# Kernel tuning notes

Measured on AMD Instinct MI355X. Metric: run time of the kernel, lower is better.

The kernel has to match this reference:

```python
import jax, jax.numpy as jnp
import numpy as np

IN_SIZE = 128
OUT_SIZE = 128
N = IN_SIZE * OUT_SIZE  # num_nets = 16384
H = 5                   # subnetwork hidden width
B = 2048                # batch


def setup_inputs() -> dict:
    key = jax.random.key(0)
    k_x, k0, k1, k2 = jax.random.split(key, 4)
    x = jax.random.normal(k_x, (B, IN_SIZE), dtype=jnp.float32)
    # init scaling mirrors _init_scaled_weights: std*0.1, last layer uses in_dim*input_size
    s0 = np.float32(np.sqrt(2.0 / 1.0) * 0.1)
    s1 = np.float32(np.sqrt(2.0 / H) * 0.1)
    s2 = np.float32(np.sqrt(2.0 / (H * IN_SIZE)) * 0.1)
    W0 = jax.random.normal(k0, (N, H, 1), dtype=jnp.float32) * s0
    W1 = jax.random.normal(k1, (N, H, H), dtype=jnp.float32) * s1
    W2 = jax.random.normal(k2, (N, 1, H), dtype=jnp.float32) * s2
    b0 = jnp.zeros((N, H, 1), dtype=jnp.float32)
    b1 = jnp.zeros((N, H, 1), dtype=jnp.float32)
    b2 = jnp.zeros((N, 1, 1), dtype=jnp.float32)
    return {"x": x, "W0": W0, "b0": b0, "W1": W1, "b1": b1, "W2": W2, "b2": b2}


def reference(x, W0, b0, W1, b1, W2, b2):
    bsz = x.shape[0]
    # x.T repeat_interleave(output_size, dim=0).unsqueeze(1): (N, 1, B)
    h = jnp.repeat(x.T, OUT_SIZE, axis=0)[:, None, :]
    h = jax.nn.silu(jnp.einsum('noi,nib->nob', W0, h) + b0)  # (N, H, B)
    h = jax.nn.silu(jnp.einsum('noi,nib->nob', W1, h) + b1)  # (N, H, B)
    h = jnp.einsum('noi,nib->nob', W2, h) + b2               # (N, 1, B)
    h = h.reshape(IN_SIZE, OUT_SIZE, bsz)
    return h.sum(axis=0).T  # (B, OUT_SIZE)
```

## Files before the change

kernel.cpp:

```cpp
#include <hip/hip_runtime.h>
#include <math.h>

#define H 5
#define IN_SIZE 128
#define OUT_SIZE 128
#define BATCH 2048

#define DEG 20
#define NC (DEG + 1)
#define KNOD 32
#define ARANGE 5.5f
#define AINV (1.0f / 5.5f)

#define KROW 2816
#define WS_MFMA ((size_t)OUT_SIZE * KROW * 2)

#define CPAD 2816
#define WS_F32 ((size_t)IN_SIZE * CPAD * sizeof(float))

typedef __attribute__((ext_vector_type(8))) short bf16x8;
typedef __attribute__((ext_vector_type(4))) float f32x4;

__device__ __forceinline__ unsigned short f2bf(float f) {
    unsigned int u = __float_as_uint(f);
    return (unsigned short)((u + 0x7FFF + ((u >> 16) & 1)) >> 16);
}
__device__ __forceinline__ unsigned int packbf(float lo, float hi) {
    return (unsigned int)f2bf(lo) | ((unsigned int)f2bf(hi) << 16);
}

__global__ __launch_bounds__(256, 4) void fit_bf16_kernel(
    const float* __restrict__ W0, const float* __restrict__ b0,
    const float* __restrict__ W1, const float* __restrict__ b1,
    const float* __restrict__ W2, const float* __restrict__ b2,
    unsigned short* __restrict__ ct, float* __restrict__ out)
{
    __shared__ float sw[368];
    __shared__ float ybuf[8][KNOD];
    const int tid = threadIdx.x;
    const int n0  = blockIdx.x * 8;

    if (tid < 128)
        out[(size_t)blockIdx.x * 128 + tid] = 0.0f;

    for (int idx = tid; idx < 368; idx += 256) {
        float v;
        if      (idx <  40) v = W0[n0 * 5  + idx];
        else if (idx <  80) v = b0[n0 * 5  + (idx - 40)];
        else if (idx < 280) v = W1[n0 * 25 + (idx - 80)];
        else if (idx < 320) v = b1[n0 * 5  + (idx - 280)];
        else if (idx < 360) v = W2[n0 * 5  + (idx - 320)];
        else                v = b2[n0 + (idx - 360)];
        sw[idx] = v;
    }
    __syncthreads();

    const int net8 = tid >> 5;
    const int k    = tid & 31;
    const int n    = n0 + net8;
    const float* w0r = sw + net8 * 5;
    const float* b0r = sw + 40  + net8 * 5;
    const float* w1r = sw + 80  + net8 * 25;
    const float* b1r = sw + 280 + net8 * 5;
    const float* w2r = sw + 320 + net8 * 5;
    const float  b2s = sw[360 + net8];

    const float theta = (k + 0.5f) * (float)(M_PI / KNOD);
    const float xv = ARANGE * __cosf(theta);

    float h1[H];
    #pragma unroll
    for (int j = 0; j < H; ++j) {
        float p = fmaf(w0r[j], xv, b0r[j]);
        h1[j] = p / (1.0f + __expf(-p));
    }
    float h2[H];
    #pragma unroll
    for (int kk = 0; kk < H; ++kk) {
        float p = b1r[kk];
        #pragma unroll
        for (int j = 0; j < H; ++j)
            p = fmaf(w1r[kk * H + j], h1[j], p);
        h2[kk] = p / (1.0f + __expf(-p));
    }
    float y = b2s;
    #pragma unroll
    for (int kk = 0; kk < H; ++kk)
        y = fmaf(w2r[kk], h2[kk], y);

    ybuf[net8][k] = y;
    __syncthreads();

    const int i = n >> 7;
    const int o = n & 127;
    if (k < NC) {
        float s = 0.0f;
        for (int kk = 0; kk < KNOD; ++kk) {
            float ang = (float)k * ((kk + 0.5f) * (float)(M_PI / KNOD));
            s += ybuf[net8][kk] * __cosf(ang);
        }
        s *= (k == 0) ? (1.0f / KNOD) : (2.0f / KNOD);
        ct[(size_t)o * KROW + i * 22 + k] = f2bf(s);
    } else if (k == NC) {
        ct[(size_t)o * KROW + i * 22 + NC] = 0;
    }
}

#define LDB 360

__global__ __launch_bounds__(256, 2) void gemm_fused_kernel(
    const float* __restrict__ x,
    const unsigned short* __restrict__ Ct,
    float* __restrict__ out)
{
    __shared__ __align__(16) unsigned short Bs[64 * LDB];
    __shared__ __align__(16) unsigned short As[32 * LDB];

    const int tid = threadIdx.x;
    const int mt = blockIdx.x;
    const int oh = blockIdx.y;
    const int bb = mt * 32;

    const int lane = tid & 63, w = tid >> 6;
    const int wm = w >> 1, wn = w & 1;
    const int l16 = lane & 15, lg = lane >> 4;

    const unsigned short* aptr  = As + (wm * 16 + l16) * LDB + lg * 8;
    const unsigned short* bptr0 = Bs + (wn * 32 + l16) * LDB + lg * 8;
    const unsigned short* bptr1 = bptr0 + 16 * LDB;

    f32x4 acc0 = {0.f, 0.f, 0.f, 0.f};
    f32x4 acc1 = {0.f, 0.f, 0.f, 0.f};

    #pragma unroll
    for (int s = 0; s < 2; ++s) {
        const int kz = blockIdx.z * 2 + s;
        const int kbase = kz * 352;
        const int i0 = kz * 16;

        if (s) __syncthreads();

        {
            const int o = tid >> 2, c = tid & 3;
            const unsigned short* src = Ct + (size_t)(oh * 64 + o) * KROW + kbase;
            unsigned short* drow = Bs + o * LDB;
            #pragma unroll
            for (int j = 0; j < 11; ++j) {
                const int kloc = c * 88 + j * 8;
                *(float4*)(drow + kloc) = *(const float4*)(src + kloc);
            }
        }

        {
            const int b  = tid & 31;
            const int s0 = tid >> 5;
            unsigned int* A32 = (unsigned int*)(As + b * LDB);
            #pragma unroll
            for (int q = 0; q < 2; ++q) {
                const int iloc = s0 + q * 8;
                const float t = x[(size_t)(bb + b) * IN_SIZE + i0 + iloc] * AINV;
                float Tv[NC];
                Tv[0] = 1.0f;
                Tv[1] = t;
                const float t2 = t + t;
                #pragma unroll
                for (int k = 2; k < NC; ++k)
                    Tv[k] = fmaf(t2, Tv[k - 1], -Tv[k - 2]);
                unsigned int* dst = A32 + iloc * 11;
                #pragma unroll
                for (int j = 0; j < 10; ++j)
                    dst[j] = packbf(Tv[2 * j], Tv[2 * j + 1]);
                dst[10] = packbf(Tv[20], 0.0f);
            }
        }
        __syncthreads();

        #pragma unroll
        for (int ks = 0; ks < 11; ++ks) {
            bf16x8 a   = *(const bf16x8*)(aptr  + ks * 32);
            bf16x8 b0v = *(const bf16x8*)(bptr0 + ks * 32);
            bf16x8 b1v = *(const bf16x8*)(bptr1 + ks * 32);
            acc0 = __builtin_amdgcn_mfma_f32_16x16x32_bf16(a, b0v, acc0, 0, 0, 0);
            acc1 = __builtin_amdgcn_mfma_f32_16x16x32_bf16(a, b1v, acc1, 0, 0, 0);
        }
    }

    const int orow = bb + wm * 16 + lg * 4;
    const int ocol = oh * 64 + wn * 32 + l16;
    #pragma unroll
    for (int r = 0; r < 4; ++r) {
        atomicAdd(&out[(size_t)(orow + r) * OUT_SIZE + ocol],      acc0[r]);
        atomicAdd(&out[(size_t)(orow + r) * OUT_SIZE + ocol + 16], acc1[r]);
    }
}

__global__ __launch_bounds__(256, 4) void fit_kernel(
    const float* __restrict__ W0, const float* __restrict__ b0,
    const float* __restrict__ W1, const float* __restrict__ b1,
    const float* __restrict__ W2, const float* __restrict__ b2,
    float* __restrict__ coef)
{
    __shared__ float sw[368];
    __shared__ float ybuf[8][KNOD];
    const int tid = threadIdx.x;
    const int n0  = blockIdx.x * 8;

    for (int idx = tid; idx < 368; idx += 256) {
        float v;
        if      (idx <  40) v = W0[n0 * 5  + idx];
        else if (idx <  80) v = b0[n0 * 5  + (idx - 40)];
        else if (idx < 280) v = W1[n0 * 25 + (idx - 80)];
        else if (idx < 320) v = b1[n0 * 5  + (idx - 280)];
        else if (idx < 360) v = W2[n0 * 5  + (idx - 320)];
        else                v = b2[n0 + (idx - 360)];
        sw[idx] = v;
    }
    __syncthreads();

    const int net8 = tid >> 5;
    const int k    = tid & 31;
    const int n    = n0 + net8;
    const float* w0r = sw + net8 * 5;
    const float* b0r = sw + 40  + net8 * 5;
    const float* w1r = sw + 80  + net8 * 25;
    const float* b1r = sw + 280 + net8 * 5;
    const float* w2r = sw + 320 + net8 * 5;
    const float  b2s = sw[360 + net8];

    const float theta = (k + 0.5f) * (float)(M_PI / KNOD);
    const float xv = ARANGE * __cosf(theta);

    float h1[H];
    #pragma unroll
    for (int j = 0; j < H; ++j) {
        float p = fmaf(w0r[j], xv, b0r[j]);
        h1[j] = p / (1.0f + __expf(-p));
    }
    float h2[H];
    #pragma unroll
    for (int kk = 0; kk < H; ++kk) {
        float p = b1r[kk];
        #pragma unroll
        for (int j = 0; j < H; ++j)
            p = fmaf(w1r[kk * H + j], h1[j], p);
        h2[kk] = p / (1.0f + __expf(-p));
    }
    float y = b2s;
    #pragma unroll
    for (int kk = 0; kk < H; ++kk)
        y = fmaf(w2r[kk], h2[kk], y);

    ybuf[net8][k] = y;
    __syncthreads();

    const int i = n >> 7;
    const int o = n & 127;
    if (k < NC) {
        float s = 0.0f;
        for (int kk = 0; kk < KNOD; ++kk) {
            float ang = (float)k * ((kk + 0.5f) * (float)(M_PI / KNOD));
            s += ybuf[net8][kk] * __cosf(ang);
        }
        s *= (k == 0) ? (1.0f / KNOD) : (2.0f / KNOD);
        coef[(size_t)i * CPAD + k * OUT_SIZE + o] = s;
    } else if (k == NC) {
        coef[(size_t)i * CPAD + NC * OUT_SIZE + o] = 0.0f;
    }
}

__global__ __launch_bounds__(256, 2) void eval_kernel(
    const float* __restrict__ x, const float* __restrict__ coef,
    float* __restrict__ out)
{
    __shared__ __align__(16) float A[16 * NC * 32];
    __shared__ __align__(16) float Bb[2][CPAD];

    const int tid = threadIdx.x;
    const int bb  = blockIdx.x * 32;
    const int i0  = blockIdx.y * 16;

    {
        const int b  = tid & 31;
        const int s0 = tid >> 5;
        #pragma unroll
        for (int q = 0; q < 2; ++q) {
            const int isub = s0 + q * 8;
            float t  = x[(size_t)(bb + b) * IN_SIZE + i0 + isub] * AINV;
            float t2 = t + t;
            float* ap = A + (isub * NC) * 32 + b;
            float Tm = 1.0f, Tc = t;
            ap[0]  = 1.0f;
            ap[32] = t;
            #pragma unroll
            for (int k = 2; k < NC; ++k) {
                float Tn = fmaf(t2, Tc, -Tm);
                Tm = Tc; Tc = Tn;
                ap[k * 32] = Tn;
            }
        }
    }

    float r[11];
    {
        const float* cb = coef + (size_t)i0 * CPAD;
        #pragma unroll
        for (int j = 0; j < 11; ++j) r[j] = cb[tid + 256 * j];
        #pragma unroll
        for (int j = 0; j < 11; ++j) Bb[0][tid + 256 * j] = r[j];
    }
    __syncthreads();

    const int w  = tid >> 6;
    const int ty = (tid >> 3) & 7;
    const int tx = tid & 7;
    const int rb = ty * 4;
    const int ob = w * 32 + tx * 4;

    float acc[4][4] = {};

    #pragma unroll 1
    for (int isub = 0; isub < 16; ++isub) {
        const int cur = isub & 1;
        if (isub + 1 < 16) {
            const float* cb = coef + (size_t)(i0 + isub + 1) * CPAD;
            #pragma unroll
            for (int j = 0; j < 11; ++j) r[j] = cb[tid + 256 * j];
        }
        const float* Ab = A + (isub * NC) * 32;
        const float* Bp = Bb[cur];
        #pragma unroll
        for (int k = 0; k < NC; ++k) {
            float4 a4 = *(const float4*)(Ab + k * 32 + rb);
            float4 b4 = *(const float4*)(Bp + k * OUT_SIZE + ob);
            float av[4] = {a4.x, a4.y, a4.z, a4.w};
            float bv[4] = {b4.x, b4.y, b4.z, b4.w};
            #pragma unroll
            for (int rr = 0; rr < 4; ++rr)
                #pragma unroll
                for (int cc = 0; cc < 4; ++cc)
                    acc[rr][cc] = fmaf(av[rr], bv[cc], acc[rr][cc]);
        }
        if (isub + 1 < 16) {
            float* Bn = Bb[cur ^ 1];
            #pragma unroll
            for (int j = 0; j < 11; ++j) Bn[tid + 256 * j] = r[j];
        }
        __syncthreads();
    }

    #pragma unroll
    for (int rr = 0; rr < 4; ++rr) {
        float* orow = out + (size_t)(bb + rb + rr) * OUT_SIZE + ob;
        #pragma unroll
        for (int cc = 0; cc < 4; ++cc)
            atomicAdd(&orow[cc], acc[rr][cc]);
    }
}

#define ICHUNK 64
#define WSTRIDE 52

__device__ __forceinline__ float silu9(float p) {
    const float c3 = -0.33333333333333f;
    const float c5 =  0.13333333333333f;
    const float c7 = -0.05396825396825f;
    const float c9 =  0.02186948853616f;
    float u  = 0.5f * p;
    float uc = fminf(fmaxf(u, -1.25f), 1.25f);
    float t  = uc * uc;
    float g  = fmaf(t, c9, c7);
    g = fmaf(t, g, c5);
    g = fmaf(t, g, c3);
    g = fmaf(t, g, 1.0f);
    return fmaf(u, uc * g, u);
}
__device__ __forceinline__ float silu5(float p) {
    const float c3 = -0.33333333333333f;
    const float c5 =  0.13333333333333f;
    float u = 0.5f * p;
    float t = u * u;
    float g = fmaf(t, c5, c3);
    g = fmaf(t, g, 1.0f);
    return fmaf(u, u * g, u);
}

__global__ __launch_bounds__(256, 8) void mlpkan_fallback(
    const float* __restrict__ x,
    const float* __restrict__ W0, const float* __restrict__ b0,
    const float* __restrict__ W1, const float* __restrict__ b1,
    const float* __restrict__ W2, const float* __restrict__ b2,
    float* __restrict__ out)
{
    __shared__ float w[ICHUNK * WSTRIDE];
    const int o  = blockIdx.x;
    const int i0 = blockIdx.z * ICHUNK;

    for (int idx = threadIdx.x; idx < ICHUNK * WSTRIDE; idx += 256) {
        int il = idx / WSTRIDE;
        int f  = idx - il * WSTRIDE;
        int n  = (i0 + il) * OUT_SIZE + o;
        float v = 0.0f;
        if (f < 5)                   v = W0[n * 5 + f];
        else if (f < 10)             v = b0[n * 5 + (f - 5)];
        else if (f >= 12 && f < 37)  v = W1[n * 25 + (f - 12)];
        else if (f >= 37 && f < 42)  v = b1[n * 5 + (f - 37)];
        else if (f >= 44 && f < 49)  v = W2[n * 5 + (f - 44)];
        else if (f == 49)            v = b2[n];
        w[idx] = v;
    }
    __syncthreads();

    const int b = blockIdx.y * 256 + threadIdx.x;
    const float* xrow = x + b * IN_SIZE + i0;
    float acc = 0.0f;

    #pragma unroll 1
    for (int i = 0; i < ICHUNK; i += 4) {
        float4 xv = *(const float4*)(xrow + i);
        float xs[4] = {xv.x, xv.y, xv.z, xv.w};
        #pragma unroll
        for (int ii = 0; ii < 4; ++ii) {
            const float4* q = (const float4*)(w + (i + ii) * WSTRIDE);
            const float xi = xs[ii];
            float g0[12];
            #pragma unroll
            for (int t = 0; t < 3; ++t) *(float4*)(g0 + 4 * t) = q[t];
            float h1[H];
            #pragma unroll
            for (int j = 0; j < H; ++j)
                h1[j] = silu9(fmaf(g0[j], xi, g0[5 + j]));
            float g1[32];
            #pragma unroll
            for (int t = 0; t < 8; ++t) *(float4*)(g1 + 4 * t) = q[3 + t];
            float h2[H];
            #pragma unroll
            for (int k = 0; k < H; ++k) {
                float p = g1[25 + k];
                #pragma unroll
                for (int j = 0; j < H; ++j)
                    p = fmaf(g1[5 * k + j], h1[j], p);
                h2[k] = silu5(p);
            }
            float g2[8];
            #pragma unroll
            for (int t = 0; t < 2; ++t) *(float4*)(g2 + 4 * t) = q[11 + t];
            float y = g2[5];
            #pragma unroll
            for (int k = 0; k < H; ++k)
                y = fmaf(g2[k], h2[k], y);
            acc += y;
        }
    }
    atomicAdd(&out[b * OUT_SIZE + o], acc);
}

extern "C" void kernel_launch(void* const* d_in, const int* in_sizes, int n_in,
                              void* d_out, int out_size, void* d_ws, size_t ws_size,
                              hipStream_t stream) {
    const float* x  = (const float*)d_in[0];
    const float* W0 = (const float*)d_in[1];
    const float* b0 = (const float*)d_in[2];
    const float* W1 = (const float*)d_in[3];
    const float* b1 = (const float*)d_in[4];
    const float* W2 = (const float*)d_in[5];
    const float* b2 = (const float*)d_in[6];
    float* out = (float*)d_out;

    if (ws_size >= WS_MFMA && d_ws != nullptr) {
        unsigned short* Ct = (unsigned short*)d_ws;
        fit_bf16_kernel<<<dim3(IN_SIZE * OUT_SIZE / 8), dim3(256), 0, stream>>>(
            W0, b0, W1, b1, W2, b2, Ct, out);
        gemm_fused_kernel<<<dim3(BATCH / 32, 2, 4), dim3(256), 0, stream>>>(
            x, Ct, out);
    } else if (ws_size >= WS_F32 && d_ws != nullptr) {
        float* coef = (float*)d_ws;
        hipMemsetAsync(out, 0, (size_t)out_size * sizeof(float), stream);
        fit_kernel<<<dim3(IN_SIZE * OUT_SIZE / 8), dim3(256), 0, stream>>>(
            W0, b0, W1, b1, W2, b2, coef);
        eval_kernel<<<dim3(BATCH / 32, IN_SIZE / 16), dim3(256), 0, stream>>>(
            x, coef, out);
    } else {
        hipMemsetAsync(out, 0, (size_t)out_size * sizeof(float), stream);
        dim3 grid(OUT_SIZE, BATCH / 256, IN_SIZE / ICHUNK);
        mlpkan_fallback<<<grid, dim3(256), 0, stream>>>(x, W0, b0, W1, b1, W2, b2, out);
    }
}
```

Baseline: 81.63 us.

## Fuse Chebyshev fit and MFMA GEMM into one cooperative kernel with grid sync

Combines the per-net Chebyshev coefficient fit and the bf16 MFMA GEMM into a single cooperative kernel, with a grid-wide barrier between the two phases and a union of their shared-memory buffers. Each of the 512 blocks now fits 32 nets instead of 8 and zeroes its slice of the output, so the second kernel launch and the gap between launches go away. In exchange the fit phase runs on far fewer blocks with more serial work per block, it depends on all 512 blocks being co-resident for the grid sync, and it falls back to the two-kernel path if the cooperative launch fails.

Result: slower. 242.7 us (+197.3%).

```diff
diff --git a/kernel.cpp b/kernel.cpp
--- a/kernel.cpp
+++ b/kernel.cpp
@@ -1,5 +1,8 @@
 #include <hip/hip_runtime.h>
+#include <hip/hip_cooperative_groups.h>
 #include <math.h>
+
+namespace cg = cooperative_groups;
 
 #define H 5
 #define IN_SIZE 128
@@ -18,6 +21,8 @@
 #define CPAD 2816
 #define WS_F32 ((size_t)IN_SIZE * CPAD * sizeof(float))
 
+#define LDB 360
+
 typedef __attribute__((ext_vector_type(8))) short bf16x8;
 typedef __attribute__((ext_vector_type(4))) float f32x4;
 
@@ -27,6 +32,180 @@
 }
 __device__ __forceinline__ unsigned int packbf(float lo, float hi) {
     return (unsigned int)f2bf(lo) | ((unsigned int)f2bf(hi) << 16);
+}
+
+union SharedU {
+    struct { unsigned short Bs[64 * LDB]; unsigned short As[32 * LDB]; } g;
+    struct { float sw[32 * 46]; float ybuf[8][KNOD]; } f;
+};
+
+__global__ __launch_bounds__(256, 2) void fused_all_kernel(
+    const float* __restrict__ x,
+    const float* __restrict__ W0, const float* __restrict__ b0,
+    const float* __restrict__ W1, const float* __restrict__ b1,
+    const float* __restrict__ W2, const float* __restrict__ b2,
+    unsigned short* ct, float* out)
+{
+    __shared__ SharedU shm;
+    const int tid = threadIdx.x;
+    const int blk = blockIdx.x + 64 * blockIdx.y + 128 * blockIdx.z;
+
+    {
+        if (tid < 128) {
+            float4 z = make_float4(0.f, 0.f, 0.f, 0.f);
+            *(float4*)(out + (size_t)blk * 512 + tid * 4) = z;
+        }
+
+        const int n0 = blk * 32;
+        for (int idx = tid; idx < 32 * 46; idx += 256) {
+            const int nl = idx / 46, f = idx - nl * 46;
+            const int n = n0 + nl;
+            float v;
+            if      (f <  5) v = W0[n * 5  + f];
+            else if (f < 10) v = b0[n * 5  + (f - 5)];
+            else if (f < 35) v = W1[n * 25 + (f - 10)];
+            else if (f < 40) v = b1[n * 5  + (f - 35)];
+            else if (f < 45) v = W2[n * 5  + (f - 40)];
+            else             v = b2[n];
+            shm.f.sw[idx] = v;
+        }
+        __syncthreads();
+
+        const int net8 = tid >> 5;
+        const int k    = tid & 31;
+        const float theta = (k + 0.5f) * (float)(M_PI / KNOD);
+        const float xv = ARANGE * __cosf(theta);
+
+        #pragma unroll 1
+        for (int q = 0; q < 4; ++q) {
+            const int nl = q * 8 + net8;
+            const float* wp = shm.f.sw + nl * 46;
+
+            float h1[H];
+            #pragma unroll
+            for (int j = 0; j < H; ++j) {
+                float p = fmaf(wp[j], xv, wp[5 + j]);
+                h1[j] = p / (1.0f + __expf(-p));
+            }
+            float h2[H];
+            #pragma unroll
+            for (int kk = 0; kk < H; ++kk) {
+                float p = wp[35 + kk];
+                #pragma unroll
+                for (int j = 0; j < H; ++j)
+                    p = fmaf(wp[10 + kk * 5 + j], h1[j], p);
+                h2[kk] = p / (1.0f + __expf(-p));
+            }
+            float y = wp[45];
+            #pragma unroll
+            for (int kk = 0; kk < H; ++kk)
+                y = fmaf(wp[40 + kk], h2[kk], y);
+
+            __syncthreads();
+            shm.f.ybuf[net8][k] = y;
+            __syncthreads();
+
+            const int n = n0 + nl;
+            const int i = n >> 7;
+            const int o = n & 127;
+            if (k < NC) {
+                float s = 0.0f;
+                for (int kk = 0; kk < KNOD; ++kk) {
+                    float ang = (float)k * ((kk + 0.5f) * (float)(M_PI / KNOD));
+                    s += shm.f.ybuf[net8][kk] * __cosf(ang);
+                }
+                s *= (k == 0) ? (1.0f / KNOD) : (2.0f / KNOD);
+                ct[(size_t)o * KROW + i * 22 + k] = f2bf(s);
+            } else if (k == NC) {
+                ct[(size_t)o * KROW + i * 22 + NC] = 0;
+            }
+        }
+    }
+
+    __threadfence();
+    cg::this_grid().sync();
+    __threadfence();
+
+    {
+        const int mt = blockIdx.x;
+        const int oh = blockIdx.y;
+        const int bb = mt * 32;
+
+        const int lane = tid & 63, w = tid >> 6;
+        const int wm = w >> 1, wn = w & 1;
+        const int l16 = lane & 15, lg = lane >> 4;
+
+        unsigned short* Bs = shm.g.Bs;
+        unsigned short* As = shm.g.As;
+
+        const unsigned short* aptr  = As + (wm * 16 + l16) * LDB + lg * 8;
+        const unsigned short* bptr0 = Bs + (wn * 32 + l16) * LDB + lg * 8;
+        const unsigned short* bptr1 = bptr0 + 16 * LDB;
+
+        f32x4 acc0 = {0.f, 0.f, 0.f, 0.f};
+        f32x4 acc1 = {0.f, 0.f, 0.f, 0.f};
+
+        #pragma unroll
+        for (int s = 0; s < 2; ++s) {
+            const int kz = blockIdx.z * 2 + s;
+            const int kbase = kz * 352;
+            const int i0 = kz * 16;
+
+            __syncthreads();
+
+            {
+                const int o = tid >> 2, c = tid & 3;
+                const unsigned short* src = ct + (size_t)(oh * 64 + o) * KROW + kbase;
+                unsigned short* drow = Bs + o * LDB;
+                #pragma unroll
+                for (int j = 0; j < 11; ++j) {
+                    const int kloc = c * 88 + j * 8;
+                    *(float4*)(drow + kloc) = *(const float4*)(src + kloc);
+                }
+            }
+
+            {
+                const int b  = tid & 31;
+                const int s0 = tid >> 5;
+                unsigned int* A32 = (unsigned int*)(As + b * LDB);
+                #pragma unroll
+                for (int q = 0; q < 2; ++q) {
+                    const int iloc = s0 + q * 8;
+                    const float t = x[(size_t)(bb + b) * IN_SIZE + i0 + iloc] * AINV;
+                    float Tv[NC];
+                    Tv[0] = 1.0f;
+                    Tv[1] = t;
+                    const float t2 = t + t;
+                    #pragma unroll
+                    for (int k = 2; k < NC; ++k)
+                        Tv[k] = fmaf(t2, Tv[k - 1], -Tv[k - 2]);
+                    unsigned int* dst = A32 + iloc * 11;
+                    #pragma unroll
+                    for (int j = 0; j < 10; ++j)
+                        dst[j] = packbf(Tv[2 * j], Tv[2 * j + 1]);
+                    dst[10] = packbf(Tv[20], 0.0f);
+                }
+            }
+            __syncthreads();
+
+            #pragma unroll
+            for (int ks = 0; ks < 11; ++ks) {
+                bf16x8 a   = *(const bf16x8*)(aptr  + ks * 32);
+                bf16x8 b0v = *(const bf16x8*)(bptr0 + ks * 32);
+                bf16x8 b1v = *(const bf16x8*)(bptr1 + ks * 32);
+                acc0 = __builtin_amdgcn_mfma_f32_16x16x32_bf16(a, b0v, acc0, 0, 0, 0);
+                acc1 = __builtin_amdgcn_mfma_f32_16x16x32_bf16(a, b1v, acc1, 0, 0, 0);
+            }
+        }
+
+        const int orow = bb + wm * 16 + lg * 4;
+        const int ocol = oh * 64 + wn * 32 + l16;
+        #pragma unroll
+        for (int r = 0; r < 4; ++r) {
+            atomicAdd(&out[(size_t)(orow + r) * OUT_SIZE + ocol],      acc0[r]);
+            atomicAdd(&out[(size_t)(orow + r) * OUT_SIZE + ocol + 16], acc1[r]);
+        }
+    }
 }
 
 __global__ __launch_bounds__(256, 4) void fit_bf16_kernel(
@@ -105,8 +284,6 @@
         ct[(size_t)o * KROW + i * 22 + NC] = 0;
     }
 }
-
-#define LDB 360
 
 __global__ __launch_bounds__(256, 2) void gemm_fused_kernel(
     const float* __restrict__ x,
@@ -468,10 +645,18 @@
 
     if (ws_size >= WS_MFMA && d_ws != nullptr) {
         unsigned short* Ct = (unsigned short*)d_ws;
-        fit_bf16_kernel<<<dim3(IN_SIZE * OUT_SIZE / 8), dim3(256), 0, stream>>>(
-            W0, b0, W1, b1, W2, b2, Ct, out);
-        gemm_fused_kernel<<<dim3(BATCH / 32, 2, 4), dim3(256), 0, stream>>>(
-            x, Ct, out);
+        dim3 grid(BATCH / 32, 2, 4);
+        dim3 block(256);
+        void* args[] = {(void*)&x, (void*)&W0, (void*)&b0, (void*)&W1, (void*)&b1,
+                        (void*)&W2, (void*)&b2, (void*)&Ct, (void*)&out};
+        hipError_t err = hipLaunchCooperativeKernel(
+            (const void*)fused_all_kernel, grid, block, args, 0, stream);
+        if (err != hipSuccess) {
+            fit_bf16_kernel<<<dim3(IN_SIZE * OUT_SIZE / 8), dim3(256), 0, stream>>>(
+                W0, b0, W1, b1, W2, b2, Ct, out);
+            gemm_fused_kernel<<<dim3(BATCH / 32, 2, 4), dim3(256), 0, stream>>>(
+                x, Ct, out);
+        }
     } else if (ws_size >= WS_F32 && d_ws != nullptr) {
         float* coef = (float*)d_ws;
         hipMemsetAsync(out, 0, (size_t)out_size * sizeof(float), stream);
```
